# Kernel optimization log

Measured on AMD Instinct MI355X. Metric: run time of the kernel, lower is better.

Reference implementation:

```python
import math
import jax, jax.numpy as jnp
import numpy as np

COLORS = 10
MAX_SHIFT = 5
B, H, W = 32, 128, 128

_shifts = [(dy, dx) for dy in range(-MAX_SHIFT, MAX_SHIFT + 1)
           for dx in range(-MAX_SHIFT, MAX_SHIFT + 1)
           if not (dy == 0 and dx == 0)]  # include_identity=False
DYS = jnp.asarray(np.array([s[0] for s in _shifts], dtype=np.int32))
DXS = jnp.asarray(np.array([s[1] for s in _shifts], dtype=np.int32))


def _shift_all(grid):
    """Apply every (dy,dx) shift to an int grid [B,H,W] with zero padding.

    out[s, b, y, x] = grid[b, y-dy_s, x-dx_s] if in-bounds else 0,
    exactly matching apply_shift_batch (uncovered regions are color 0).
    Returns [S, B, H, W].
    """
    b, h, w = grid.shape
    padded = jnp.pad(grid, ((0, 0), (MAX_SHIFT, MAX_SHIFT), (MAX_SHIFT, MAX_SHIFT)))
    def one(dy, dx):
        return jax.lax.dynamic_slice(padded, (0, MAX_SHIFT - dy, MAX_SHIFT - dx), (b, h, w))
    return jax.vmap(one)(DYS, DXS)


def setup_inputs() -> dict:
    key = jax.random.key(0)
    k1, k2, k3 = jax.random.split(key, 3)
    return {
        "demo_in": jax.random.randint(k1, (B, H, W), 0, COLORS, dtype=jnp.int32),
        "demo_out": jax.random.randint(k2, (B, H, W), 0, COLORS, dtype=jnp.int32),
        "query_in": jax.random.randint(k3, (B, H, W), 0, COLORS, dtype=jnp.int32),
        "color_log_weight": jnp.zeros((COLORS,), dtype=jnp.float32),
        "logit_scale": jnp.asarray(4.0, dtype=jnp.float32),
    }


def reference(demo_in, demo_out, query_in, color_log_weight, logit_scale):
    b, h, w = query_in.shape
    S = DYS.shape[0]

    # Per-shift correlation score. one_hot(shifted)*one_hot(demo_out)*w summed
    # over (C,H,W) == sum over pixels of w[demo_out] * (shifted == demo_out).
    shifted_demo = _shift_all(demo_in)                       # [S,B,H,W] int
    w_out = jnp.exp(color_log_weight)[demo_out]              # [B,H,W]
    eq = (shifted_demo == demo_out[None]).astype(jnp.float32)
    match = jnp.sum(eq * w_out[None], axis=(2, 3))           # [S,B]
    scale = jnp.minimum(jnp.exp(logit_scale), 100.0)
    scores = match.T / math.sqrt(h * w) * scale              # [B,S]
    attention = jax.nn.softmax(scores, axis=1)               # [B,S]

    # Weighted accumulation of one-hot shifted queries, done as a scatter-add
    # into the color channel (avoids materializing [S,B,C,H,W]).
    shifted_query = _shift_all(query_in)                     # [S,B,H,W] int
    b_idx = jnp.arange(b)[None, :, None, None]
    y_idx = jnp.arange(h)[None, None, :, None]
    x_idx = jnp.arange(w)[None, None, None, :]
    attn_b = jnp.broadcast_to(attention.T[:, :, None, None], (S, b, h, w))
    accum = jnp.zeros((b, COLORS, h, w), dtype=jnp.float32)
    accum = accum.at[b_idx, shifted_query, y_idx, x_idx].add(attn_b)
    return jnp.log(jnp.maximum(accum, 1e-6))
```

## Files before the change

### kernel.cpp

```cpp
#include <hip/hip_runtime.h>
#include <hip/hip_bf16.h>
#include <math.h>

#define COLORS 10
#define NB 32
#define H 128
#define W 128
#define NS 120
#define HW (H*W)
#define STRIPS 8
#define SH 16
#define DROWS 26
#define DINW 12
#define AR 18

typedef unsigned char u8;
typedef unsigned int u32;
typedef unsigned long long u64;
typedef float f32x4 __attribute__((ext_vector_type(4)));
typedef short bf16x8 __attribute__((ext_vector_type(8)));

__global__ __launch_bounds__(512) void match_strip(
    const int* __restrict__ demo_in, const int* __restrict__ demo_out,
    const float* __restrict__ clw, float* __restrict__ mpart)
{
    __shared__ __align__(16) u32 din_p[COLORS][DROWS][DINW];
    __shared__ __align__(16) u32 dout_p[COLORS][SH][4];
    __shared__ float wexp[COLORS];

    int t = threadIdx.x;
    int strip = blockIdx.x;
    int b = blockIdx.y;
    int wave = t >> 6, lane = t & 63;
    int y0 = strip * SH;

    if (t < COLORS) wexp[t] = __expf(clw[t]);

    const int* di = demo_in  + b * HW;
    const int* dd = demo_out + b * HW;

    for (int r = wave; r < DROWS; r += 8) {
        int gy = y0 - 5 + r;
        bool ok = (gy >= 0 && gy < H);
        int v0 = 0, v1 = 0;
        if (ok) { v0 = di[gy * W + lane]; v1 = di[gy * W + 64 + lane]; }
        #pragma unroll
        for (int c = 0; c < COLORS; c++) {
            u64 h0 = __ballot(v0 == c);
            u64 h1 = __ballot(v1 == c);
            u64 P0, P1, P2;
            if (!ok) {
                P0 = (c == 0) ? ~0ull : 0ull;
                P1 = P0;
                P2 = (c == 0) ? 0x3FFull : 0ull;
            } else {
                u64 lm = (c == 0) ? 0x1Full  : 0ull;
                u64 rm = (c == 0) ? 0x3E0ull : 0ull;
                P0 = (h0 << 5) | lm;
                P1 = (h0 >> 59) | (h1 << 5);
                P2 = (h1 >> 59) | rm;
            }
            if (lane == 0) {
                *reinterpret_cast<uint4*>(&din_p[c][r][0]) =
                    make_uint4((u32)P0, (u32)(P0 >> 32), (u32)P1, (u32)(P1 >> 32));
                *reinterpret_cast<uint4*>(&din_p[c][r][4]) =
                    make_uint4((u32)P2, 0u, 0u, 0u);
            }
        }
    }
    for (int r = wave; r < SH; r += 8) {
        int gy = y0 + r;
        int v0 = dd[gy * W + lane], v1 = dd[gy * W + 64 + lane];
        #pragma unroll
        for (int c = 0; c < COLORS; c++) {
            u64 h0 = __ballot(v0 == c);
            u64 h1 = __ballot(v1 == c);
            if (lane == 0)
                *reinterpret_cast<uint4*>(&dout_p[c][r][0]) =
                    make_uint4((u32)h0, (u32)(h0 >> 32), (u32)h1, (u32)(h1 >> 32));
        }
    }
    __syncthreads();

    float acc[11];
    #pragma unroll
    for (int i = 0; i < 11; i++) acc[i] = 0.f;

    if (t < 352) {
        int dyIdx = t >> 5;
        int ch    = (t >> 4) & 1;
        int y     = t & 15;
        int r     = y - dyIdx + 10;

        #pragma unroll
        for (int cc = 0; cc < 5; cc++) {
            int c = ch * 5 + cc;
            const u32* dr = &din_p[c][r][0];
            u32 d0 = dr[0], d1 = dr[1], d2 = dr[2], d3 = dr[3], d4 = dr[4];
            const u32* orw = &dout_p[c][y][0];
            u32 o0 = orw[0], o1 = orw[1], o2 = orw[2], o3 = orw[3];
            float wgt = wexp[c];
            #pragma unroll
            for (int dxi = 0; dxi < 11; dxi++) {
                int k = 10 - dxi;
                u32 s0 = __builtin_amdgcn_alignbit(d1, d0, k);
                u32 s1 = __builtin_amdgcn_alignbit(d2, d1, k);
                u32 s2 = __builtin_amdgcn_alignbit(d3, d2, k);
                u32 s3 = __builtin_amdgcn_alignbit(d4, d3, k);
                int cnt = __popc(s0 & o0) + __popc(s1 & o1)
                        + __popc(s2 & o2) + __popc(s3 & o3);
                acc[dxi] += wgt * (float)cnt;
            }
        }
    }

    #pragma unroll
    for (int dxi = 0; dxi < 11; dxi++) {
        float v = acc[dxi];
        v += __shfl_down(v, 16, 32);
        v += __shfl_down(v, 8, 32);
        v += __shfl_down(v, 4, 32);
        v += __shfl_down(v, 2, 32);
        v += __shfl_down(v, 1, 32);
        acc[dxi] = v;
    }
    if ((t & 31) == 0 && t < 352) {
        int dyIdx = t >> 5;
        #pragma unroll
        for (int dxi = 0; dxi < 11; dxi++) {
            int lin = dyIdx * 11 + dxi;
            if (lin == 60) continue;
            int s = lin - (lin > 60);
            mpart[(b * NS + s) * STRIPS + strip] = acc[dxi];
        }
    }
}

__global__ __launch_bounds__(512) void accum_fused(
    const int* __restrict__ query_in, const float* __restrict__ mpart,
    const float* __restrict__ logit_scale, float* __restrict__ out)
{
    __shared__ u8  qs[AR][144];
    __shared__ float sm[NS];
    __shared__ unsigned short abf[128];
    __shared__ __align__(16) u32 Agl[11][64][4];

    int t  = threadIdx.x;
    int y0 = blockIdx.x * 8;
    int b  = blockIdx.y;
    const int* q = query_in + b * HW;

    u32 pk0 = 0, pk1 = 0;
    {
        int g = t;
        #pragma unroll
        for (int e = 0; e < 4; e++) {
            int idx = g * 4 + e;
            int r = idx / 144, p = idx - r * 144;
            int gy = y0 - 5 + r;
            bool ok = (gy >= 0) & (gy < H) & (p >= 5) & (p < 133);
            int cy = gy < 0 ? 0 : (gy > 127 ? 127 : gy);
            int cx = p < 5 ? 0 : (p > 132 ? 127 : p - 5);
            int v = q[cy * W + cx];
            pk0 |= (u32)(ok ? v : 0) << (8 * e);
        }
    }
    if (t < 648 - 512) {
        int g = t + 512;
        #pragma unroll
        for (int e = 0; e < 4; e++) {
            int idx = g * 4 + e;
            int r = idx / 144, p = idx - r * 144;
            int gy = y0 - 5 + r;
            bool ok = (gy >= 0) & (gy < H) & (p >= 5) & (p < 133);
            int cy = gy < 0 ? 0 : (gy > 127 ? 127 : gy);
            int cx = p < 5 ? 0 : (p > 132 ? 127 : p - 5);
            int v = q[cy * W + cx];
            pk1 |= (u32)(ok ? v : 0) << (8 * e);
        }
    }

    float scale = fminf(__expf(logit_scale[0]), 100.0f) * (1.0f / 128.0f);
    if (t < NS) {
        const float* mp = mpart + (t + b * NS) * STRIPS;
        float4 v0 = *reinterpret_cast<const float4*>(mp);
        float4 v1 = *reinterpret_cast<const float4*>(mp + 4);
        sm[t] = (v0.x + v0.y + v0.z + v0.w + v1.x + v1.y + v1.z + v1.w) * scale;
    }

    ((u32*)qs)[t] = pk0;
    if (t < 648 - 512) ((u32*)qs)[t + 512] = pk1;
    __syncthreads();

    if (t < 64) {
        float s0 = sm[t];
        float s1 = (t + 64 < NS) ? sm[t + 64] : -INFINITY;
        float m = fmaxf(s0, s1);
        for (int off = 32; off > 0; off >>= 1) m = fmaxf(m, __shfl_xor(m, off, 64));
        float e0 = __expf(s0 - m);
        float e1 = (t + 64 < NS) ? __expf(s1 - m) : 0.f;
        float sum = e0 + e1;
        for (int off = 32; off > 0; off >>= 1) sum += __shfl_xor(sum, off, 64);
        float inv = 1.0f / sum;
        sm[t] = e0 * inv;
        if (t + 64 < NS) sm[t + 64] = e1 * inv;
    }
    __syncthreads();
    if (t < 128) {
        unsigned short v = 0;
        if (t < 121 && t != 60) {
            int si = t - (t > 60);
            __hip_bfloat16 hb = __float2bfloat16(sm[si]);
            v = *reinterpret_cast<unsigned short*>(&hb);
        }
        abf[t] = v;
    }
    __syncthreads();

    {
        int e = t;
        int st = e >> 6, l = e & 63;
        int mrow = l & 15, g8 = (l >> 4) * 8;
        #pragma unroll
        for (int p = 0; p < 4; p++) {
            int j0 = mrow + 10 - (g8 + p * 2);
            int j1 = j0 - 1;
            int i0 = (j0 >= 0 && j0 <= 10) ? (10 - st) * 11 + j0 : 121;
            int i1 = (j1 >= 0 && j1 <= 10) ? (10 - st) * 11 + j1 : 121;
            Agl[st][l][p] = (u32)abf[i0] | ((u32)abf[i1] << 16);
        }
    }
    if (t < 704 - 512) {
        int e = t + 512;
        int st = e >> 6, l = e & 63;
        int mrow = l & 15, g8 = (l >> 4) * 8;
        #pragma unroll
        for (int p = 0; p < 4; p++) {
            int j0 = mrow + 10 - (g8 + p * 2);
            int j1 = j0 - 1;
            int i0 = (j0 >= 0 && j0 <= 10) ? (10 - st) * 11 + j0 : 121;
            int i1 = (j1 >= 0 && j1 <= 10) ? (10 - st) * 11 + j1 : 121;
            Agl[st][l][p] = (u32)abf[i0] | ((u32)abf[i1] << 16);
        }
    }
    __syncthreads();

    int lane = t & 63, w = t >> 6;
    int x0 = w * 16;
    int c = lane & 15, g = lane >> 4;

    #define BUILD_B(r) ({                                                        \
        u64 eight = *reinterpret_cast<const u64*>(&qs[(r)][x0 + 8 * g]);         \
        u32 lo = (u32)eight, hi = (u32)(eight >> 32);                            \
        u32 b0 = ((int)(lo & 255) == c ? 0x3F80u : 0u)                           \
               | ((int)((lo >> 8)  & 255) == c ? 0x3F800000u : 0u);              \
        u32 b1 = ((int)((lo >> 16) & 255) == c ? 0x3F80u : 0u)                   \
               | ((int)((lo >> 24) & 255) == c ? 0x3F800000u : 0u);              \
        u32 b2 = ((int)(hi & 255) == c ? 0x3F80u : 0u)                           \
               | ((int)((hi >> 8)  & 255) == c ? 0x3F800000u : 0u);              \
        u32 b3 = ((int)((hi >> 16) & 255) == c ? 0x3F80u : 0u)                   \
               | ((int)((hi >> 24) & 255) == c ? 0x3F800000u : 0u);              \
        make_uint4(b0, b1, b2, b3); })

    uint4 bf[8];
    #pragma unroll
    for (int r = 0; r < 7; r++) bf[r & 7] = BUILD_B(r);

    f32x4 acc0[4], acc1[4];
    #pragma unroll
    for (int j = 0; j < 4; j++) { acc0[j] = (f32x4){0,0,0,0}; acc1[j] = (f32x4){0,0,0,0}; }

    #pragma unroll
    for (int st = 0; st < 11; st++) {
        bf[(st + 7) & 7] = BUILD_B(st + 7);
        uint4 a4 = *reinterpret_cast<const uint4*>(&Agl[st][lane][0]);
        union { uint4 u; bf16x8 v; } A; A.u = a4;
        #pragma unroll
        for (int j = 0; j < 4; j++) {
            union { uint4 u; bf16x8 v; } B0, B1;
            B0.u = bf[(st + j) & 7];
            B1.u = bf[(st + 4 + j) & 7];
            acc0[j] = __builtin_amdgcn_mfma_f32_16x16x32_bf16(A.v, B0.v, acc0[j], 0, 0, 0);
            acc1[j] = __builtin_amdgcn_mfma_f32_16x16x32_bf16(A.v, B1.v, acc1[j], 0, 0, 0);
        }
    }
    #undef BUILD_B

    if (c < COLORS) {
        #pragma unroll
        for (int j = 0; j < 4; j++) {
            float* ob0 = out + (((size_t)b * COLORS + c) * H + (y0 + j)) * W + x0 + 4 * g;
            float4 r0;
            r0.x = __logf(fmaxf(acc0[j][0], 1e-6f));
            r0.y = __logf(fmaxf(acc0[j][1], 1e-6f));
            r0.z = __logf(fmaxf(acc0[j][2], 1e-6f));
            r0.w = __logf(fmaxf(acc0[j][3], 1e-6f));
            *reinterpret_cast<float4*>(ob0) = r0;
            float* ob1 = out + (((size_t)b * COLORS + c) * H + (y0 + 4 + j)) * W + x0 + 4 * g;
            float4 r1;
            r1.x = __logf(fmaxf(acc1[j][0], 1e-6f));
            r1.y = __logf(fmaxf(acc1[j][1], 1e-6f));
            r1.z = __logf(fmaxf(acc1[j][2], 1e-6f));
            r1.w = __logf(fmaxf(acc1[j][3], 1e-6f));
            *reinterpret_cast<float4*>(ob1) = r1;
        }
    }
}

__global__ __launch_bounds__(256) void match_kernel(
    const int* __restrict__ demo_in, const int* __restrict__ demo_out,
    const float* __restrict__ clw, float* __restrict__ match)
{
    int blk = blockIdx.x;
    int b = blk / NS;
    int s = blk % NS;
    int lin = s + (s >= 60 ? 1 : 0);
    int dy = lin / 11 - 5, dx = lin % 11 - 5;

    __shared__ float wexp[COLORS];
    int tid = threadIdx.x;
    if (tid < COLORS) wexp[tid] = expf(clw[tid]);
    __syncthreads();

    const int* __restrict__ din  = demo_in  + b * HW;
    const int* __restrict__ dout = demo_out + b * HW;

    float partial = 0.f;
    for (int i = tid; i < HW; i += 256) {
        int yy = i >> 7, xx = i & 127;
        int co = dout[i];
        int sy = yy - dy, sx = xx - dx;
        int v = 0;
        if (sy >= 0 && sy < H && sx >= 0 && sx < W) v = din[sy * W + sx];
        if (v == co) partial += wexp[co];
    }
    for (int off = 32; off > 0; off >>= 1) partial += __shfl_down(partial, off, 64);
    __shared__ float wsum[4];
    if ((tid & 63) == 0) wsum[tid >> 6] = partial;
    __syncthreads();
    if (tid == 0) match[blk] = wsum[0] + wsum[1] + wsum[2] + wsum[3];
}

__global__ __launch_bounds__(64) void softmax_kernel(
    const float* __restrict__ match, const float* __restrict__ logit_scale,
    float* __restrict__ attention)
{
    int b = blockIdx.x;
    int lane = threadIdx.x;
    float scale = fminf(expf(logit_scale[0]), 100.0f) / sqrtf((float)HW);
    int i0 = lane, i1 = lane + 64;
    float s0 = match[b * NS + i0] * scale;
    float s1 = (i1 < NS) ? match[b * NS + i1] * scale : -INFINITY;
    float m = fmaxf(s0, s1);
    for (int off = 32; off > 0; off >>= 1) m = fmaxf(m, __shfl_xor(m, off, 64));
    float e0 = expf(s0 - m);
    float e1 = (i1 < NS) ? expf(s1 - m) : 0.f;
    float sum = e0 + e1;
    for (int off = 32; off > 0; off >>= 1) sum += __shfl_xor(sum, off, 64);
    float inv = 1.0f / sum;
    attention[b * NS + i0] = e0 * inv;
    if (i1 < NS) attention[b * NS + i1] = e1 * inv;
}

__global__ __launch_bounds__(128) void accum_kernel(
    const int* __restrict__ query_in, const float* __restrict__ attention,
    float* __restrict__ out)
{
    int blk = blockIdx.x;
    int b = blk >> 7;
    int y = blk & 127;
    int x = threadIdx.x;

    __shared__ float att[NS];
    if (threadIdx.x < NS) att[threadIdx.x] = attention[b * NS + threadIdx.x];
    __syncthreads();

    const int* __restrict__ q = query_in + b * HW;
    float acc[COLORS];
    #pragma unroll
    for (int c = 0; c < COLORS; c++) acc[c] = 0.f;

    #pragma unroll 4
    for (int s = 0; s < NS; s++) {
        int lin = s + (s >= 60 ? 1 : 0);
        int dy = lin / 11 - 5, dx = lin % 11 - 5;
        int sy = y - dy, sx = x - dx;
        int v = 0;
        if (sy >= 0 && sy < H && sx >= 0 && sx < W) v = q[sy * W + sx];
        float a = att[s];
        #pragma unroll
        for (int c = 0; c < COLORS; c++) acc[c] += (v == c) ? a : 0.f;
    }
    float* __restrict__ ob = out + (size_t)b * COLORS * HW + y * W + x;
    #pragma unroll
    for (int c = 0; c < COLORS; c++) ob[c * HW] = __logf(fmaxf(acc[c], 1e-6f));
}

extern "C" void kernel_launch(void* const* d_in, const int* in_sizes, int n_in,
                              void* d_out, int out_size, void* d_ws, size_t ws_size,
                              hipStream_t stream) {
    const int*   demo_in     = (const int*)d_in[0];
    const int*   demo_out    = (const int*)d_in[1];
    const int*   query_in    = (const int*)d_in[2];
    const float* clw         = (const float*)d_in[3];
    const float* logit_scale = (const float*)d_in[4];
    float* out = (float*)d_out;

    size_t needed = (size_t)NB * NS * STRIPS * sizeof(float);

    if (ws_size >= needed) {
        float* mpart = (float*)d_ws;
        match_strip<<<dim3(STRIPS, NB), 512, 0, stream>>>(demo_in, demo_out, clw, mpart);
        accum_fused<<<dim3(H / 8, NB), 512, 0, stream>>>(query_in, mpart, logit_scale, out);
    } else {
        float* match = (float*)d_ws;
        float* att   = match + NB * NS;
        match_kernel<<<NB * NS, 256, 0, stream>>>(demo_in, demo_out, clw, match);
        softmax_kernel<<<NB, 64, 0, stream>>>(match, logit_scale, att);
        accum_kernel<<<NB * H, 128, 0, stream>>>(query_in, att, out);
    }
}
```

Measured before the change: 29.47 us.

## Halve block sizes: 16 eight-row strips for match, two tiles per wave in accum

The match kernel now uses 256-thread blocks over 16 strips of 8 rows instead of 512 threads over 8 strips of 16 rows, and writes 16 partials per shift. The accum kernel drops to 256 threads, with each wave looping over two 16-column tiles, and the attention reduction now sums 16 partials. The aim is more, smaller blocks, with launch bounds requesting 4 blocks per CU for better occupancy and latency hiding. In exchange, the match kernel recomputes more halo rows, and each accum thread does more serial work with higher register pressure.

```diff
diff --git a/kernel.cpp b/kernel.cpp
--- a/kernel.cpp
+++ b/kernel.cpp
@@ -8,9 +8,8 @@
 #define W 128
 #define NS 120
 #define HW (H*W)
-#define STRIPS 8
-#define SH 16
-#define DROWS 26
+#define NT 16
+#define DR2 18
 #define DINW 12
 #define AR 18
 
@@ -20,26 +19,26 @@
 typedef float f32x4 __attribute__((ext_vector_type(4)));
 typedef short bf16x8 __attribute__((ext_vector_type(8)));
 
-__global__ __launch_bounds__(512) void match_strip(
+__global__ __launch_bounds__(256, 4) void match_strip(
     const int* __restrict__ demo_in, const int* __restrict__ demo_out,
     const float* __restrict__ clw, float* __restrict__ mpart)
 {
-    __shared__ __align__(16) u32 din_p[COLORS][DROWS][DINW];
-    __shared__ __align__(16) u32 dout_p[COLORS][SH][4];
+    __shared__ __align__(16) u32 din_p[COLORS][DR2][DINW];
+    __shared__ __align__(16) u32 dout_p[COLORS][8][4];
     __shared__ float wexp[COLORS];
 
     int t = threadIdx.x;
     int strip = blockIdx.x;
     int b = blockIdx.y;
     int wave = t >> 6, lane = t & 63;
-    int y0 = strip * SH;
+    int y0 = strip * 8;
 
     if (t < COLORS) wexp[t] = __expf(clw[t]);
 
     const int* di = demo_in  + b * HW;
     const int* dd = demo_out + b * HW;
 
-    for (int r = wave; r < DROWS; r += 8) {
+    for (int r = wave; r < DR2; r += 4) {
         int gy = y0 - 5 + r;
         bool ok = (gy >= 0 && gy < H);
         int v0 = 0, v1 = 0;
@@ -68,7 +67,7 @@
             }
         }
     }
-    for (int r = wave; r < SH; r += 8) {
+    for (int r = wave; r < 8; r += 4) {
         int gy = y0 + r;
         int v0 = dd[gy * W + lane], v1 = dd[gy * W + 64 + lane];
         #pragma unroll
@@ -86,10 +85,10 @@
     #pragma unroll
     for (int i = 0; i < 11; i++) acc[i] = 0.f;
 
-    if (t < 352) {
-        int dyIdx = t >> 5;
-        int ch    = (t >> 4) & 1;
-        int y     = t & 15;
+    if (t < 176) {
+        int dyIdx = t >> 4;
+        int ch    = (t >> 3) & 1;
+        int y     = t & 7;
         int r     = y - dyIdx + 10;
 
         #pragma unroll
@@ -117,26 +116,25 @@
     #pragma unroll
     for (int dxi = 0; dxi < 11; dxi++) {
         float v = acc[dxi];
-        v += __shfl_down(v, 16, 32);
-        v += __shfl_down(v, 8, 32);
-        v += __shfl_down(v, 4, 32);
-        v += __shfl_down(v, 2, 32);
-        v += __shfl_down(v, 1, 32);
+        v += __shfl_down(v, 8, 16);
+        v += __shfl_down(v, 4, 16);
+        v += __shfl_down(v, 2, 16);
+        v += __shfl_down(v, 1, 16);
         acc[dxi] = v;
     }
-    if ((t & 31) == 0 && t < 352) {
-        int dyIdx = t >> 5;
+    if ((t & 15) == 0 && t < 176) {
+        int dyIdx = t >> 4;
         #pragma unroll
         for (int dxi = 0; dxi < 11; dxi++) {
             int lin = dyIdx * 11 + dxi;
             if (lin == 60) continue;
             int s = lin - (lin > 60);
-            mpart[(b * NS + s) * STRIPS + strip] = acc[dxi];
-        }
-    }
-}
-
-__global__ __launch_bounds__(512) void accum_fused(
+            mpart[(b * NS + s) * NT + strip] = acc[dxi];
+        }
+    }
+}
+
+__global__ __launch_bounds__(256, 4) void accum_fused(
     const int* __restrict__ query_in, const float* __restrict__ mpart,
     const float* __restrict__ logit_scale, float* __restrict__ out)
 {
@@ -150,46 +148,57 @@
     int b  = blockIdx.y;
     const int* q = query_in + b * HW;
 
-    u32 pk0 = 0, pk1 = 0;
-    {
-        int g = t;
+    u32 pk0 = 0, pk1 = 0, pk2 = 0;
+    #pragma unroll
+    for (int e = 0; e < 4; e++) {
+        int idx = t * 4 + e;
+        int r = idx / 144, p = idx - r * 144;
+        int gy = y0 - 5 + r;
+        bool ok = (gy >= 0) & (gy < H) & (p >= 5) & (p < 133);
+        int cy = gy < 0 ? 0 : (gy > 127 ? 127 : gy);
+        int cx = p < 5 ? 0 : (p > 132 ? 127 : p - 5);
+        int v = q[cy * W + cx];
+        pk0 |= (u32)(ok ? v : 0) << (8 * e);
+    }
+    #pragma unroll
+    for (int e = 0; e < 4; e++) {
+        int idx = (t + 256) * 4 + e;
+        int r = idx / 144, p = idx - r * 144;
+        int gy = y0 - 5 + r;
+        bool ok = (gy >= 0) & (gy < H) & (p >= 5) & (p < 133);
+        int cy = gy < 0 ? 0 : (gy > 127 ? 127 : gy);
+        int cx = p < 5 ? 0 : (p > 132 ? 127 : p - 5);
+        int v = q[cy * W + cx];
+        pk1 |= (u32)(ok ? v : 0) << (8 * e);
+    }
+    if (t < 648 - 512) {
         #pragma unroll
         for (int e = 0; e < 4; e++) {
-            int idx = g * 4 + e;
+            int idx = (t + 512) * 4 + e;
             int r = idx / 144, p = idx - r * 144;
             int gy = y0 - 5 + r;
             bool ok = (gy >= 0) & (gy < H) & (p >= 5) & (p < 133);
             int cy = gy < 0 ? 0 : (gy > 127 ? 127 : gy);
             int cx = p < 5 ? 0 : (p > 132 ? 127 : p - 5);
             int v = q[cy * W + cx];
-            pk0 |= (u32)(ok ? v : 0) << (8 * e);
-        }
-    }
-    if (t < 648 - 512) {
-        int g = t + 512;
-        #pragma unroll
-        for (int e = 0; e < 4; e++) {
-            int idx = g * 4 + e;
-            int r = idx / 144, p = idx - r * 144;
-            int gy = y0 - 5 + r;
-            bool ok = (gy >= 0) & (gy < H) & (p >= 5) & (p < 133);
-            int cy = gy < 0 ? 0 : (gy > 127 ? 127 : gy);
-            int cx = p < 5 ? 0 : (p > 132 ? 127 : p - 5);
-            int v = q[cy * W + cx];
-            pk1 |= (u32)(ok ? v : 0) << (8 * e);
+            pk2 |= (u32)(ok ? v : 0) << (8 * e);
         }
     }
 
     float scale = fminf(__expf(logit_scale[0]), 100.0f) * (1.0f / 128.0f);
     if (t < NS) {
-        const float* mp = mpart + (t + b * NS) * STRIPS;
+        const float* mp = mpart + (t + b * NS) * NT;
         float4 v0 = *reinterpret_cast<const float4*>(mp);
         float4 v1 = *reinterpret_cast<const float4*>(mp + 4);
-        sm[t] = (v0.x + v0.y + v0.z + v0.w + v1.x + v1.y + v1.z + v1.w) * scale;
+        float4 v2 = *reinterpret_cast<const float4*>(mp + 8);
+        float4 v3 = *reinterpret_cast<const float4*>(mp + 12);
+        sm[t] = (v0.x + v0.y + v0.z + v0.w + v1.x + v1.y + v1.z + v1.w
+               + v2.x + v2.y + v2.z + v2.w + v3.x + v3.y + v3.z + v3.w) * scale;
     }
 
     ((u32*)qs)[t] = pk0;
-    if (t < 648 - 512) ((u32*)qs)[t + 512] = pk1;
+    ((u32*)qs)[t + 256] = pk1;
+    if (t < 648 - 512) ((u32*)qs)[t + 512] = pk2;
     __syncthreads();
 
     if (t < 64) {
@@ -217,40 +226,29 @@
     }
     __syncthreads();
 
-    {
-        int e = t;
-        int st = e >> 6, l = e & 63;
-        int mrow = l & 15, g8 = (l >> 4) * 8;
-        #pragma unroll
-        for (int p = 0; p < 4; p++) {
-            int j0 = mrow + 10 - (g8 + p * 2);
-            int j1 = j0 - 1;
-            int i0 = (j0 >= 0 && j0 <= 10) ? (10 - st) * 11 + j0 : 121;
-            int i1 = (j1 >= 0 && j1 <= 10) ? (10 - st) * 11 + j1 : 121;
-            Agl[st][l][p] = (u32)abf[i0] | ((u32)abf[i1] << 16);
-        }
-    }
-    if (t < 704 - 512) {
-        int e = t + 512;
-        int st = e >> 6, l = e & 63;
-        int mrow = l & 15, g8 = (l >> 4) * 8;
-        #pragma unroll
-        for (int p = 0; p < 4; p++) {
-            int j0 = mrow + 10 - (g8 + p * 2);
-            int j1 = j0 - 1;
-            int i0 = (j0 >= 0 && j0 <= 10) ? (10 - st) * 11 + j0 : 121;
-            int i1 = (j1 >= 0 && j1 <= 10) ? (10 - st) * 11 + j1 : 121;
-            Agl[st][l][p] = (u32)abf[i0] | ((u32)abf[i1] << 16);
+    #pragma unroll
+    for (int base = 0; base < 768; base += 256) {
+        int e = t + base;
+        if (e < 704) {
+            int st = e >> 6, l = e & 63;
+            int mrow = l & 15, g8 = (l >> 4) * 8;
+            #pragma unroll
+            for (int p = 0; p < 4; p++) {
+                int j0 = mrow + 10 - (g8 + p * 2);
+                int j1 = j0 - 1;
+                int i0 = (j0 >= 0 && j0 <= 10) ? (10 - st) * 11 + j0 : 121;
+                int i1 = (j1 >= 0 && j1 <= 10) ? (10 - st) * 11 + j1 : 121;
+                Agl[st][l][p] = (u32)abf[i0] | ((u32)abf[i1] << 16);
+            }
         }
     }
     __syncthreads();
 
     int lane = t & 63, w = t >> 6;
-    int x0 = w * 16;
     int c = lane & 15, g = lane >> 4;
 
-    #define BUILD_B(r) ({                                                        \
-        u64 eight = *reinterpret_cast<const u64*>(&qs[(r)][x0 + 8 * g]);         \
+    #define BUILD_B(r, x0) ({                                                    \
+        u64 eight = *reinterpret_cast<const u64*>(&qs[(r)][(x0) + 8 * g]);       \
         u32 lo = (u32)eight, hi = (u32)(eight >> 32);                            \
         u32 b0 = ((int)(lo & 255) == c ? 0x3F80u : 0u)                           \
                | ((int)((lo >> 8)  & 255) == c ? 0x3F800000u : 0u);              \
@@ -262,49 +260,54 @@
                | ((int)((hi >> 24) & 255) == c ? 0x3F800000u : 0u);              \
         make_uint4(b0, b1, b2, b3); })
 
-    uint4 bf[8];
-    #pragma unroll
-    for (int r = 0; r < 7; r++) bf[r & 7] = BUILD_B(r);
-
-    f32x4 acc0[4], acc1[4];
-    #pragma unroll
-    for (int j = 0; j < 4; j++) { acc0[j] = (f32x4){0,0,0,0}; acc1[j] = (f32x4){0,0,0,0}; }
-
-    #pragma unroll
-    for (int st = 0; st < 11; st++) {
-        bf[(st + 7) & 7] = BUILD_B(st + 7);
-        uint4 a4 = *reinterpret_cast<const uint4*>(&Agl[st][lane][0]);
-        union { uint4 u; bf16x8 v; } A; A.u = a4;
-        #pragma unroll
-        for (int j = 0; j < 4; j++) {
-            union { uint4 u; bf16x8 v; } B0, B1;
-            B0.u = bf[(st + j) & 7];
-            B1.u = bf[(st + 4 + j) & 7];
-            acc0[j] = __builtin_amdgcn_mfma_f32_16x16x32_bf16(A.v, B0.v, acc0[j], 0, 0, 0);
-            acc1[j] = __builtin_amdgcn_mfma_f32_16x16x32_bf16(A.v, B1.v, acc1[j], 0, 0, 0);
+    #pragma unroll
+    for (int ti = 0; ti < 2; ti++) {
+        int x0 = (w * 2 + ti) * 16;
+
+        uint4 bf[8];
+        #pragma unroll
+        for (int r = 0; r < 7; r++) bf[r & 7] = BUILD_B(r, x0);
+
+        f32x4 acc0[4], acc1[4];
+        #pragma unroll
+        for (int j = 0; j < 4; j++) { acc0[j] = (f32x4){0,0,0,0}; acc1[j] = (f32x4){0,0,0,0}; }
+
+        #pragma unroll
+        for (int st = 0; st < 11; st++) {
+            bf[(st + 7) & 7] = BUILD_B(st + 7, x0);
+            uint4 a4 = *reinterpret_cast<const uint4*>(&Agl[st][lane][0]);
+            union { uint4 u; bf16x8 v; } A; A.u = a4;
+            #pragma unroll
+            for (int j = 0; j < 4; j++) {
+                union { uint4 u; bf16x8 v; } B0, B1;
+                B0.u = bf[(st + j) & 7];
+                B1.u = bf[(st + 4 + j) & 7];
+                acc0[j] = __builtin_amdgcn_mfma_f32_16x16x32_bf16(A.v, B0.v, acc0[j], 0, 0, 0);
+                acc1[j] = __builtin_amdgcn_mfma_f32_16x16x32_bf16(A.v, B1.v, acc1[j], 0, 0, 0);
+            }
+        }
+
+        if (c < COLORS) {
+            #pragma unroll
+            for (int j = 0; j < 4; j++) {
+                float* ob0 = out + (((size_t)b * COLORS + c) * H + (y0 + j)) * W + x0 + 4 * g;
+                float4 r0;
+                r0.x = __logf(fmaxf(acc0[j][0], 1e-6f));
+                r0.y = __logf(fmaxf(acc0[j][1], 1e-6f));
+                r0.z = __logf(fmaxf(acc0[j][2], 1e-6f));
+                r0.w = __logf(fmaxf(acc0[j][3], 1e-6f));
+                *reinterpret_cast<float4*>(ob0) = r0;
+                float* ob1 = out + (((size_t)b * COLORS + c) * H + (y0 + 4 + j)) * W + x0 + 4 * g;
+                float4 r1;
+                r1.x = __logf(fmaxf(acc1[j][0], 1e-6f));
+                r1.y = __logf(fmaxf(acc1[j][1], 1e-6f));
+                r1.z = __logf(fmaxf(acc1[j][2], 1e-6f));
+                r1.w = __logf(fmaxf(acc1[j][3], 1e-6f));
+                *reinterpret_cast<float4*>(ob1) = r1;
+            }
         }
     }
     #undef BUILD_B
-
-    if (c < COLORS) {
-        #pragma unroll
-        for (int j = 0; j < 4; j++) {
-            float* ob0 = out + (((size_t)b * COLORS + c) * H + (y0 + j)) * W + x0 + 4 * g;
-            float4 r0;
-            r0.x = __logf(fmaxf(acc0[j][0], 1e-6f));
-            r0.y = __logf(fmaxf(acc0[j][1], 1e-6f));
-            r0.z = __logf(fmaxf(acc0[j][2], 1e-6f));
-            r0.w = __logf(fmaxf(acc0[j][3], 1e-6f));
-            *reinterpret_cast<float4*>(ob0) = r0;
-            float* ob1 = out + (((size_t)b * COLORS + c) * H + (y0 + 4 + j)) * W + x0 + 4 * g;
-            float4 r1;
-            r1.x = __logf(fmaxf(acc1[j][0], 1e-6f));
-            r1.y = __logf(fmaxf(acc1[j][1], 1e-6f));
-            r1.z = __logf(fmaxf(acc1[j][2], 1e-6f));
-            r1.w = __logf(fmaxf(acc1[j][3], 1e-6f));
-            *reinterpret_cast<float4*>(ob1) = r1;
-        }
-    }
 }
 
 __global__ __launch_bounds__(256) void match_kernel(
@@ -406,12 +409,12 @@
     const float* logit_scale = (const float*)d_in[4];
     float* out = (float*)d_out;
 
-    size_t needed = (size_t)NB * NS * STRIPS * sizeof(float);
+    size_t needed = (size_t)NB * NS * NT * sizeof(float);
 
     if (ws_size >= needed) {
         float* mpart = (float*)d_ws;
-        match_strip<<<dim3(STRIPS, NB), 512, 0, stream>>>(demo_in, demo_out, clw, mpart);
-        accum_fused<<<dim3(H / 8, NB), 512, 0, stream>>>(query_in, mpart, logit_scale, out);
+        match_strip<<<dim3(NT, NB), 256, 0, stream>>>(demo_in, demo_out, clw, mpart);
+        accum_fused<<<dim3(H / 8, NB), 256, 0, stream>>>(query_in, mpart, logit_scale, out);
     } else {
         float* match = (float*)d_ws;
         float* att   = match + NB * NS;
```

After: 47.83 us. 62.3% more time.
